# Kernel tuning notes

Measured on AMD Instinct MI355X. Metric: run time of the kernel, lower is better.

The kernel has to match this reference:

```python
import jax, jax.numpy as jnp
import numpy as np

N = 50000   # nodes
F = 32      # num_node_features
EMB = 32    # embedding_size
R = 8       # num_relations
L = 5       # num_layers
E = 400000  # edges


def setup_inputs() -> dict:
    key = jax.random.key(0)
    ks = jax.random.split(key, 12)
    s = 0.1  # weight scale ~ 1/sqrt(fan_in) for stability over 5 residual layers
    return {
        "x": jax.random.normal(ks[0], (N, F), jnp.float32),
        "edge_index": jax.random.randint(ks[1], (2, E), 0, N, jnp.int32),
        "edge_type": jax.random.randint(ks[2], (E,), 0, R, jnp.int32),
        "edge_dist": jax.random.uniform(ks[3], (E,), jnp.float32),
        "fc_W": jax.random.normal(ks[4], (F, EMB), jnp.float32) * s,
        "fc_b": jnp.zeros((EMB,), jnp.float32),
        "rgcn_W": jax.random.normal(ks[5], (L, R, EMB, EMB), jnp.float32) * s,
        "rgcn_root": jax.random.normal(ks[6], (L, EMB, EMB), jnp.float32) * s,
        "rgcn_bias": jnp.zeros((L, EMB), jnp.float32),
        "mlp_W1": jax.random.normal(ks[7], (1 + R, EMB), jnp.float32) * s,
        "mlp_b1": jnp.zeros((EMB,), jnp.float32),
        "mlp_W2": jax.random.normal(ks[8], (EMB, EMB * EMB), jnp.float32) * s,
        "mlp_b2": jnp.zeros((EMB * EMB,), jnp.float32),
        "nn_root": jax.random.normal(ks[9], (L, EMB, EMB), jnp.float32) * s,
        "nn_bias": jnp.zeros((L, EMB), jnp.float32),
    }


def _forward(x, edge_index, edge_type, edge_dist, fc_W, fc_b, rgcn_W, rgcn_root,
             rgcn_bias, mlp_W1, mlp_b1, mlp_W2, mlp_b2, nn_root, nn_bias):
    n = x.shape[0]
    src, dst = edge_index[0], edge_index[1]  # source_to_target flow

    # edge_attr_c = [distance, onehot(edge_type)] : [E, 1+R]
    onehot = jax.nn.one_hot(edge_type, R, dtype=x.dtype)
    eattr = jnp.concatenate([edge_dist[:, None], onehot], axis=1)

    # Shared edge_mlp -> per-edge [EMB, EMB] weight (same for every NNConv layer)
    We = (jax.nn.relu(eattr @ mlp_W1 + mlp_b1) @ mlp_W2 + mlp_b2).reshape(-1, EMB, EMB)

    # degree for NNConv mean aggregation
    deg = jax.ops.segment_sum(jnp.ones_like(edge_dist), dst, num_segments=n)
    denom = jnp.maximum(deg, 1.0)[:, None]

    # per-relation in-degree for RGCN per-relation mean
    rel_cnt = []
    for r in range(R):
        c = jax.ops.segment_sum((edge_type == r).astype(x.dtype), dst, num_segments=n)
        rel_cnt.append(jnp.maximum(c, 1.0)[:, None])

    h = jax.nn.relu(x @ fc_W + fc_b)
    for l in range(L):
        # RGCNConv: root transform + per-relation mean of W_r x_j
        out = h @ rgcn_root[l] + rgcn_bias[l]
        for r in range(R):
            mask_r = (edge_type == r).astype(h.dtype)[:, None]
            msg = (h @ rgcn_W[l, r])[src] * mask_r  # [E, EMB]
            out = out + jax.ops.segment_sum(msg, dst, num_segments=n) / rel_cnt[r]
        h_disc = jax.nn.relu(out)

        # NNConv: x_j @ Theta(e) per edge, mean-aggregated, + root + bias
        msg = jnp.einsum('ei,eio->eo', h[src], We)  # [E, EMB]
        agg = jax.ops.segment_sum(msg, dst, num_segments=n) / denom
        h_cont = jax.nn.relu(h @ nn_root[l] + agg + nn_bias[l])

        h = h + h_disc + h_cont
    return h


def reference(x, edge_index, edge_type, edge_dist, fc_W, fc_b, rgcn_W, rgcn_root,
              rgcn_bias, mlp_W1, mlp_b1, mlp_W2, mlp_b2, nn_root, nn_bias):
    return _forward(x, edge_index, edge_type, edge_dist, fc_W, fc_b, rgcn_W,
                    rgcn_root, rgcn_bias, mlp_W1, mlp_b1, mlp_W2, mlp_b2,
                    nn_root, nn_bias)
```

## Files before the change

### kernel.cpp

```cpp
#include <hip/hip_runtime.h>

#define N_NODES 50000
#define N_EDGES 400000
#define EMB 32
#define NREL 8
#define NLAYER 5
#define NPB 16
#define NBLK (N_NODES / NPB)
#define KROWS 43
#define NCHUNK 196
#define E2CAP (N_EDGES + 8 * N_NODES)

typedef __attribute__((ext_vector_type(8))) short short8;
typedef __attribute__((ext_vector_type(4))) float f32x4;
typedef __attribute__((ext_vector_type(4))) unsigned int u32x4v;

__device__ __forceinline__ unsigned short f2bf(float f) {
    unsigned u = __float_as_uint(f);
    unsigned r = u + 0x7FFF + ((u >> 16) & 1);
    return (unsigned short)(r >> 16);
}

__device__ __forceinline__ unsigned cvt_pk(float a, float b) {
    unsigned r;
    asm("v_cvt_pk_bf16_f32 %0, %1, %2" : "=v"(r) : "v"(a), "v"(b));
    return r;
}

__device__ __forceinline__ int pdeg_of(int d) {
    return (d > 0 ? d + 7 : 8) & ~7;
}

__device__ __forceinline__ int bkt_of(int d) {
    int b = pdeg_of(d) >> 3;
    return (b > 32 ? 32 : b) - 1;
}


__global__ __launch_bounds__(256) void fill_kernel(int* __restrict__ zeroblk,
                                                   float* __restrict__ ha,
                                                   float* __restrict__ hb) {
    int i = blockIdx.x * 256 + threadIdx.x;
    if (i < 10 * N_NODES + 64) zeroblk[i] = 0;
    if (i < EMB) { ha[(size_t)N_NODES * EMB + i] = 0.0f; hb[(size_t)N_NODES * EMB + i] = 0.0f; }
}

__global__ __launch_bounds__(256) void hist_kernel(const int* __restrict__ ei,
                                                   const int* __restrict__ et,
                                                   int* __restrict__ deg,
                                                   int* __restrict__ relcnt) {
    int e = blockIdx.x * 256 + threadIdx.x;
    if (e < N_EDGES) {
        int d = ei[N_EDGES + e];
        atomicAdd(&deg[d], 1);
        atomicAdd(&relcnt[d * NREL + et[e]], 1);
    }
}

__global__ __launch_bounds__(256) void nodeprep_kernel(const int* __restrict__ deg,
                                                       const int* __restrict__ relcnt,
                                                       int* __restrict__ bsum,
                                                       float* __restrict__ invdeg,
                                                       float* __restrict__ invcnt,
                                                       int* __restrict__ bcnt) {
    __shared__ int wsum[4];
    __shared__ int lhist[32];
    int tid = threadIdx.x, lane = tid & 63, wv = tid >> 6;
    if (tid < 32) lhist[tid] = 0;
    int i = blockIdx.x * 256 + tid;
    int d = (i < N_NODES) ? deg[i] : 0;
    int v = (i < N_NODES) ? pdeg_of(d) : 0;
    #pragma unroll
    for (int off = 32; off > 0; off >>= 1) v += __shfl_down(v, off, 64);
    if (lane == 0) wsum[wv] = v;
    __syncthreads();
    if (tid == 0) bsum[blockIdx.x] = wsum[0] + wsum[1] + wsum[2] + wsum[3];
    if (i < N_NODES) {
        invdeg[i] = 1.0f / (float)(d > 0 ? d : 1);
        #pragma unroll
        for (int r = 0; r < NREL; r++) {
            int c = relcnt[i * NREL + r];
            invcnt[i * NREL + r] = 1.0f / (float)(c > 0 ? c : 1);
        }
        atomicAdd(&lhist[bkt_of(d)], 1);
    }
    __syncthreads();
    if (tid < 32 && lhist[tid] > 0) atomicAdd(&bcnt[tid], lhist[tid]);
}

__global__ __launch_bounds__(256) void boff_kernel(const int* __restrict__ bsum,
                                                   int* __restrict__ boff,
                                                   int* __restrict__ row_ptr,
                                                   const int* __restrict__ bcnt,
                                                   int* __restrict__ bcur) {
    __shared__ int ws[4];
    int tid = threadIdx.x, lane = tid & 63, w = tid >> 6;
    int v = (tid < NCHUNK) ? bsum[tid] : 0;
    int incl = v;
    #pragma unroll
    for (int off = 1; off < 64; off <<= 1) {
        int t = __shfl_up(incl, off, 64);
        if (lane >= off) incl += t;
    }
    if (lane == 63) ws[w] = incl;
    __syncthreads();
    int add = 0;
    for (int j = 0; j < w; j++) add += ws[j];
    if (tid < NCHUNK) boff[tid] = add + incl - v;
    if (tid == 0) {
        row_ptr[N_NODES] = ws[0] + ws[1] + ws[2] + ws[3];
        int acc = 0;
        for (int b = 0; b < 32; b++) { bcur[b] = acc; acc += bcnt[b]; }
    }
}

__global__ __launch_bounds__(256) void rptr_kernel(const int* __restrict__ deg,
                                                   const int* __restrict__ boff,
                                                   int* __restrict__ row_ptr,
                                                   int* __restrict__ bcur,
                                                   int* __restrict__ sched) {
    __shared__ int ws[4];
    __shared__ int lcnt[32];
    __shared__ int lbase[32];
    int tid = threadIdx.x, lane = tid & 63, w = tid >> 6;
    if (tid < 32) lcnt[tid] = 0;
    int i = blockIdx.x * 256 + tid;
    int d = (i < N_NODES) ? deg[i] : 0;
    int v = (i < N_NODES) ? pdeg_of(d) : 0;
    int incl = v;
    #pragma unroll
    for (int off = 1; off < 64; off <<= 1) {
        int t = __shfl_up(incl, off, 64);
        if (lane >= off) incl += t;
    }
    if (lane == 63) ws[w] = incl;
    __syncthreads();
    int add = boff[blockIdx.x];
    for (int j = 0; j < w; j++) add += ws[j];
    int rank = 0, bkt = 0;
    if (i < N_NODES) {
        row_ptr[i] = add + incl - v;
        bkt = bkt_of(d);
        rank = atomicAdd(&lcnt[bkt], 1);
    }
    __syncthreads();
    if (tid < 32 && lcnt[tid] > 0) lbase[tid] = atomicAdd(&bcur[tid], lcnt[tid]);
    __syncthreads();
    if (i < N_NODES) sched[lbase[bkt] + rank] = i;
}

__global__ __launch_bounds__(256) void scatter_kernel(const int* __restrict__ ei,
                                                      const int* __restrict__ et,
                                                      const float* __restrict__ ed,
                                                      const int* __restrict__ row_ptr,
                                                      const int* __restrict__ deg,
                                                      int* __restrict__ cursor,
                                                      int2* __restrict__ edge2,
                                                      const int* __restrict__ sched,
                                                      int4* __restrict__ wavetab) {
    int e = blockIdx.x * 256 + threadIdx.x;
    if (e < N_EDGES) {
        int d = ei[N_EDGES + e];
        int pos = row_ptr[d] + atomicAdd(&cursor[d], 1);
        edge2[pos] = make_int2(ei[e] | (et[e] << 16), __float_as_int(ed[e]));
    }
    if (e < N_NODES) {
        int base = row_ptr[e], d = deg[e], pd = pdeg_of(d);
        for (int p = base + d; p < base + pd; ++p)
            edge2[p] = make_int2(N_NODES, 0);
        int node = sched[e];
        wavetab[e] = make_int4(node, row_ptr[node], pdeg_of(deg[node]), 0);
    }
}

__global__ __launch_bounds__(256) void wtbf_kernel(const float* __restrict__ W2,
                                                   const float* __restrict__ b2,
                                                   const float* __restrict__ rgcnW,
                                                   const float* __restrict__ rgcnRoot,
                                                   const float* __restrict__ nnRoot,
                                                   unsigned short* __restrict__ WB) {
    int m = blockIdx.x;
    const float* src;
    if (m < 32) src = W2 + (size_t)m * 1024;
    else if (m == 32) src = b2;
    else {
        int t = m - 33, l = t / 10, j = t % 10;
        src = (j < 8) ? rgcnW + (size_t)(l * 8 + j) * 1024
            : (j == 8) ? rgcnRoot + (size_t)l * 1024
                       : nnRoot + (size_t)l * 1024;
    }
    unsigned short* dst = WB + (size_t)m * 1024;
    #pragma unroll
    for (int c = 0; c < 4; c++) {
        int idx = c * 256 + threadIdx.x;
        int o = idx >> 5, k = idx & 31;
        int i = (k >> 1) + ((k & 1) << 4);
        dst[o * 32 + k] = f2bf(src[i * 32 + o]);
    }
}


__global__ __launch_bounds__(256) void fc_kernel(const float* __restrict__ x,
                                                 const float* __restrict__ W,
                                                 const float* __restrict__ b,
                                                 float* __restrict__ h) {
    __shared__ __align__(16) float xt[8][EMB];
    int tid = threadIdx.x;
    int nl = tid >> 5, lane = tid & 31;
    int n0 = blockIdx.x * 8;
    xt[tid >> 5][tid & 31] = x[n0 * EMB + tid];
    __syncthreads();
    float acc = b[lane];
    #pragma unroll
    for (int i = 0; i < EMB; i++) acc += xt[nl][i] * W[i * EMB + lane];
    int ol = ((lane & 15) << 1) | (lane >> 4);
    h[(n0 + nl) * EMB + ol] = fmaxf(acc, 0.0f);
}


__device__ __forceinline__ void gath(const float* __restrict__ h, int4 E, int m,
                                     float2& ga, float2& gb) {
    ga = *(const float2*)&h[((E.x & 0xFFFF) << 5) + 2 * m];
    gb = *(const float2*)&h[((E.z & 0xFFFF) << 5) + 2 * m];
}

__device__ __forceinline__ void proc_pair(int4 E, float2 ga, float2 gb,
                                          const float2* wrb2f, float w10_0, float w10_1,
                                          unsigned selm, int m,
                                          unsigned& A0s, unsigned& A1s, unsigned& ASs,
                                          unsigned& B0s, unsigned& B1s) {
    int ra = (E.x >> 16) & 7, rb = (E.z >> 16) & 7;
    float2 wa = wrb2f[ra * 16 + m];
    float2 wb = wrb2f[rb * 16 + m];
    float da = __int_as_float(E.y), db = __int_as_float(E.w);
    float hA0 = fmaxf(fmaf(da, w10_0, wa.x), 0.f);
    float hA1 = fmaxf(fmaf(da, w10_1, wa.y), 0.f);
    float hB0 = fmaxf(fmaf(db, w10_0, wb.x), 0.f);
    float hB1 = fmaxf(fmaf(db, w10_1, wb.y), 0.f);
    A0s = cvt_pk(hA0, hB0);
    A1s = cvt_pk(hA1, hB1);
    ASs = cvt_pk((float)((selm >> ra) & 1u), (float)((selm >> rb) & 1u));
    B0s = cvt_pk(ga.x, gb.x);
    B1s = cvt_pk(ga.y, gb.y);
}

__device__ __forceinline__ void mfma6(const unsigned* fa0v, const unsigned* fa1v,
                                      const unsigned* fasv, const unsigned* fb0v,
                                      const unsigned* fb1v,
                                      f32x4& aP00, f32x4& aP01, f32x4& aP10, f32x4& aP11,
                                      f32x4& aS0, f32x4& aS1) {
    u32x4v u0 = {fa0v[0], fa0v[1], fa0v[2], fa0v[3]};
    u32x4v u1 = {fa1v[0], fa1v[1], fa1v[2], fa1v[3]};
    u32x4v us = {fasv[0], fasv[1], fasv[2], fasv[3]};
    u32x4v v0 = {fb0v[0], fb0v[1], fb0v[2], fb0v[3]};
    u32x4v v1 = {fb1v[0], fb1v[1], fb1v[2], fb1v[3]};
    short8 A0 = __builtin_bit_cast(short8, u0);
    short8 A1 = __builtin_bit_cast(short8, u1);
    short8 AS = __builtin_bit_cast(short8, us);
    short8 B0 = __builtin_bit_cast(short8, v0);
    short8 B1 = __builtin_bit_cast(short8, v1);
    aP00 = __builtin_amdgcn_mfma_f32_16x16x32_bf16(A0, B0, aP00, 0, 0, 0);
    aP01 = __builtin_amdgcn_mfma_f32_16x16x32_bf16(A0, B1, aP01, 0, 0, 0);
    aP10 = __builtin_amdgcn_mfma_f32_16x16x32_bf16(A1, B0, aP10, 0, 0, 0);
    aP11 = __builtin_amdgcn_mfma_f32_16x16x32_bf16(A1, B1, aP11, 0, 0, 0);
    aS0  = __builtin_amdgcn_mfma_f32_16x16x32_bf16(AS, B0, aS0, 0, 0, 0);
    aS1  = __builtin_amdgcn_mfma_f32_16x16x32_bf16(AS, B1, aS1, 0, 0, 0);
}

__device__ __forceinline__ void edge_pass(const float* __restrict__ h,
                                          const int2* __restrict__ edge2,
                                          const float2* wrb2f,
                                          int pb, int pe, int quad, int m,
                                          float w10_0, float w10_1, unsigned selm,
                                          int4 E0, float2 g0a, float2 g0b,
                                          f32x4& aP00, f32x4& aP01, f32x4& aP10,
                                          f32x4& aP11, f32x4& aS0, f32x4& aS1) {
    {
        unsigned fa0v[4] = {0,0,0,0}, fa1v[4] = {0,0,0,0}, fasv[4] = {0,0,0,0};
        unsigned fb0v[4] = {0,0,0,0}, fb1v[4] = {0,0,0,0};
        proc_pair(E0, g0a, g0b, wrb2f, w10_0, w10_1, selm, m,
                  fa0v[0], fa1v[0], fasv[0], fb0v[0], fb1v[0]);
        if (pb + 8 < pe) {
            int4 E = *(const int4*)&edge2[pb + 8 + quad * 2];
            float2 ga, gb; gath(h, E, m, ga, gb);
            proc_pair(E, ga, gb, wrb2f, w10_0, w10_1, selm, m,
                      fa0v[1], fa1v[1], fasv[1], fb0v[1], fb1v[1]);
        }
        if (pb + 16 < pe) {
            int4 E = *(const int4*)&edge2[pb + 16 + quad * 2];
            float2 ga, gb; gath(h, E, m, ga, gb);
            proc_pair(E, ga, gb, wrb2f, w10_0, w10_1, selm, m,
                      fa0v[2], fa1v[2], fasv[2], fb0v[2], fb1v[2]);
        }
        if (pb + 24 < pe) {
            int4 E = *(const int4*)&edge2[pb + 24 + quad * 2];
            float2 ga, gb; gath(h, E, m, ga, gb);
            proc_pair(E, ga, gb, wrb2f, w10_0, w10_1, selm, m,
                      fa0v[3], fa1v[3], fasv[3], fb0v[3], fb1v[3]);
        }
        mfma6(fa0v, fa1v, fasv, fb0v, fb1v, aP00, aP01, aP10, aP11, aS0, aS1);
    }
    for (int c0 = pb + 32; c0 < pe; c0 += 32) {
        unsigned fa0v[4] = {0,0,0,0}, fa1v[4] = {0,0,0,0}, fasv[4] = {0,0,0,0};
        unsigned fb0v[4] = {0,0,0,0}, fb1v[4] = {0,0,0,0};
        #pragma unroll
        for (int jp = 0; jp < 4; ++jp) {
            if (c0 + jp * 8 < pe) {
                int4 E = *(const int4*)&edge2[c0 + jp * 8 + quad * 2];
                float2 ga, gb; gath(h, E, m, ga, gb);
                proc_pair(E, ga, gb, wrb2f, w10_0, w10_1, selm, m,
                          fa0v[jp], fa1v[jp], fasv[jp], fb0v[jp], fb1v[jp]);
            }
        }
        mfma6(fa0v, fa1v, fasv, fb0v, fb1v, aP00, aP01, aP10, aP11, aS0, aS1);
    }
}

__device__ __forceinline__ void stage_node(unsigned short (*P)[EMB], int quad, int m,
                                           float idg, const float* __restrict__ invcnt_n,
                                           const float* __restrict__ hrow,
                                           const f32x4& aP00, const f32x4& aP01,
                                           const f32x4& aP10, const f32x4& aP11,
                                           const f32x4& aS0, const f32x4& aS1) {
    #pragma unroll
    for (int reg = 0; reg < 4; ++reg) {
        const int row = quad * 4 + reg;
        *(unsigned*)&P[row][2 * m]      = cvt_pk(aP00[reg] * idg, aP01[reg] * idg);
        *(unsigned*)&P[row + 16][2 * m] = cvt_pk(aP10[reg] * idg, aP11[reg] * idg);
        if (row <= 8) {
            const float sc = (row == 0) ? idg : invcnt_n[row - 1];
            *(unsigned*)&P[32 + row][2 * m] = cvt_pk(aS0[reg] * sc, aS1[reg] * sc);
        }
    }
    if (quad < 2) {
        float2 hh = *(const float2*)&hrow[2 * m];
        *(unsigned*)&P[41 + quad][2 * m] = cvt_pk(hh.x, hh.y);
    }
}

__global__ __launch_bounds__(1024, 8) void layer_kernel(
    const float* __restrict__ h,
    const int2* __restrict__ edge2,
    const int4* __restrict__ wavetab,
    const float* __restrict__ invdeg,
    const float* __restrict__ invcnt,
    const float* __restrict__ W1,
    const float* __restrict__ b1,
    const unsigned short* __restrict__ WBs,
    const unsigned short* __restrict__ WBl,
    const float* __restrict__ rgcnBias_l,
    const float* __restrict__ nnBias_l,
    float* __restrict__ hout,
    int last)
{
    __shared__ __align__(16) unsigned short P_lds[NPB][KROWS][EMB];
    __shared__ __align__(16) float2 wrb2f[NREL * 16];
    __shared__ int nodeid[NPB];

    const int tid = threadIdx.x;

    if (tid < 128) {
        int r = tid >> 4, mi = tid & 15;
        wrb2f[r * 16 + mi] = make_float2(W1[(1 + r) * EMB + mi] + b1[mi],
                                         W1[(1 + r) * EMB + mi + 16] + b1[mi + 16]);
    }

    const int l    = tid & 63;
    const int w    = tid >> 6;
    const int quad = l >> 4;
    const int m    = l & 15;
    const float w10_0 = W1[m];
    const float w10_1 = W1[m + 16];
    const unsigned selm = (m == 0) ? 0xFFu : (m <= 8 ? (1u << (m - 1)) : 0u);

    int4 wt = wavetab[blockIdx.x * NPB + w];
    const int node = wt.x, pb = wt.y, pe = wt.y + wt.z;
    if (l == 0) nodeid[w] = node;
    int4 E0 = *(const int4*)&edge2[pb + quad * 2];
    float2 g0a, g0b;
    gath(h, E0, m, g0a, g0b);

    __syncthreads();

    {
        f32x4 aP00 = {0,0,0,0}, aP01 = {0,0,0,0}, aP10 = {0,0,0,0}, aP11 = {0,0,0,0};
        f32x4 aS0 = {0,0,0,0}, aS1 = {0,0,0,0};
        edge_pass(h, edge2, wrb2f, pb, pe, quad, m, w10_0, w10_1, selm,
                  E0, g0a, g0b, aP00, aP01, aP10, aP11, aS0, aS1);
        stage_node(P_lds[w], quad, m, invdeg[node], invcnt + (size_t)node * NREL,
                   h + (size_t)node * EMB, aP00, aP01, aP10, aP11, aS0, aS1);
    }
    __syncthreads();

    const int node16 = l & 15;
    const int o0 = l & 15;

    f32x4 accN0 = {0,0,0,0}, accN1 = {0,0,0,0};
    f32x4 accR0 = {0,0,0,0}, accR1 = {0,0,0,0};

    #pragma unroll
    for (int j = 0; j < 3; j++) {
        const int rr = w + 16 * j;
        if (rr < KROWS) {
            const unsigned short* Bsrc = (rr < 33) ? (WBs + (size_t)rr * 1024)
                                                   : (WBl + (size_t)(rr - 33) * 1024);
            short8 bf0 = *(const short8*)(Bsrc + o0 * 32 + quad * 8);
            short8 bf1 = *(const short8*)(Bsrc + (o0 + 16) * 32 + quad * 8);
            short8 a = *(const short8*)&P_lds[node16][rr][quad * 8];
            if (rr <= 32 || rr == 42) {
                accN0 = __builtin_amdgcn_mfma_f32_16x16x32_bf16(a, bf0, accN0, 0, 0, 0);
                accN1 = __builtin_amdgcn_mfma_f32_16x16x32_bf16(a, bf1, accN1, 0, 0, 0);
            } else {
                accR0 = __builtin_amdgcn_mfma_f32_16x16x32_bf16(a, bf0, accR0, 0, 0, 0);
                accR1 = __builtin_amdgcn_mfma_f32_16x16x32_bf16(a, bf1, accR1, 0, 0, 0);
            }
        }
    }
    __syncthreads();

    float* RedAll = (float*)&P_lds[0][0][0];
    if (w < 8) {
        float* my = RedAll + w * 1024;
        #pragma unroll
        for (int reg = 0; reg < 4; reg++) {
            int nd = quad * 4 + reg;
            my[nd * 32 + o0]            = accN0[reg];
            my[nd * 32 + o0 + 16]       = accN1[reg];
            my[512 + nd * 32 + o0]      = accR0[reg];
            my[512 + nd * 32 + o0 + 16] = accR1[reg];
        }
    }
    __syncthreads();
    if (w >= 8) {
        float* my = RedAll + (w - 8) * 1024;
        #pragma unroll
        for (int reg = 0; reg < 4; reg++) {
            int nd = quad * 4 + reg;
            my[nd * 32 + o0]            += accN0[reg];
            my[nd * 32 + o0 + 16]       += accN1[reg];
            my[512 + nd * 32 + o0]      += accR0[reg];
            my[512 + nd * 32 + o0 + 16] += accR1[reg];
        }
    }
    __syncthreads();

    if (tid < 512) {
        const int hw2 = tid >> 5, lane = tid & 31;
        const int n2 = nodeid[hw2];
        float sn = 0.0f, sr = 0.0f;
        #pragma unroll
        for (int ww = 0; ww < 8; ww++) {
            sn += RedAll[ww * 1024 + tid];
            sr += RedAll[ww * 1024 + 512 + tid];
        }
        const int il = ((lane & 15) << 1) | (lane >> 4);
        float hd = h[(size_t)n2 * EMB + il];
        float o_r = fmaxf(sr + rgcnBias_l[lane], 0.0f);
        float o_n = fmaxf(sn + nnBias_l[lane], 0.0f);
        hout[(size_t)n2 * EMB + (last ? lane : il)] = hd + o_r + o_n;
    }
}


extern "C" void kernel_launch(void* const* d_in, const int* in_sizes, int n_in,
                              void* d_out, int out_size, void* d_ws, size_t ws_size,
                              hipStream_t stream) {
    const float* x        = (const float*)d_in[0];
    const int*   ei       = (const int*)d_in[1];
    const int*   et       = (const int*)d_in[2];
    const float* ed       = (const float*)d_in[3];
    const float* fcW      = (const float*)d_in[4];
    const float* fcb      = (const float*)d_in[5];
    const float* rgcnW    = (const float*)d_in[6];
    const float* rgcnRoot = (const float*)d_in[7];
    const float* rgcnBias = (const float*)d_in[8];
    const float* W1       = (const float*)d_in[9];
    const float* b1       = (const float*)d_in[10];
    const float* W2       = (const float*)d_in[11];
    const float* b2       = (const float*)d_in[12];
    const float* nnRoot   = (const float*)d_in[13];
    const float* nnBias   = (const float*)d_in[14];

    float* ws = (float*)d_ws;
    float* h_a    = ws;  ws += (size_t)(N_NODES + 1) * EMB;
    float* h_b    = ws;  ws += (size_t)(N_NODES + 1) * EMB;
    float* invdeg = ws;  ws += (size_t)N_NODES;
    float* invcnt = ws;  ws += (size_t)N_NODES * NREL;
    unsigned short* WB = (unsigned short*)ws;  ws += (size_t)83 * 1024 / 2;
    int2* edge2   = (int2*)ws;     ws += (size_t)E2CAP * 2;
    int* row_ptr  = (int*)ws;      ws += (size_t)(N_NODES + 1);
    int* bsum     = (int*)ws;      ws += (size_t)NCHUNK;
    int* boff     = (int*)ws;      ws += (size_t)NCHUNK;
    int* deg      = (int*)ws;      ws += (size_t)N_NODES;
    int* relcnt   = (int*)ws;      ws += (size_t)N_NODES * NREL;
    int* cursor   = (int*)ws;      ws += (size_t)N_NODES;
    int* bcnt     = (int*)ws;      ws += 32;
    int* bcur     = (int*)ws;      ws += 32;
    int* sched    = (int*)ws;      ws += (size_t)N_NODES;
    int4* wavetab = (int4*)ws;     ws += (size_t)N_NODES * 4;
    (void)in_sizes; (void)n_in; (void)out_size; (void)ws_size;

    fill_kernel<<<(10 * N_NODES + 64 + 255) / 256, 256, 0, stream>>>(deg, h_a, h_b);
    hist_kernel<<<(N_EDGES + 255) / 256, 256, 0, stream>>>(ei, et, deg, relcnt);
    nodeprep_kernel<<<NCHUNK, 256, 0, stream>>>(deg, relcnt, bsum, invdeg, invcnt, bcnt);
    boff_kernel<<<1, 256, 0, stream>>>(bsum, boff, row_ptr, bcnt, bcur);
    rptr_kernel<<<NCHUNK, 256, 0, stream>>>(deg, boff, row_ptr, bcur, sched);
    scatter_kernel<<<(N_EDGES + 255) / 256, 256, 0, stream>>>(ei, et, ed, row_ptr, deg,
                                                              cursor, edge2, sched, wavetab);
    wtbf_kernel<<<83, 256, 0, stream>>>(W2, b2, rgcnW, rgcnRoot, nnRoot, WB);
    fc_kernel<<<N_NODES / 8, 256, 0, stream>>>(x, fcW, fcb, h_a);

    const float* hin = h_a;
    float* houtb = h_b;
    for (int l = 0; l < NLAYER; l++) {
        float* dst = (l == NLAYER - 1) ? (float*)d_out : houtb;
        layer_kernel<<<NBLK, 1024, 0, stream>>>(
            hin, edge2, wavetab, invdeg, invcnt, W1, b1,
            WB, WB + (size_t)(33 + l * 10) * 1024,
            rgcnBias + (size_t)l * EMB,
            nnBias + (size_t)l * EMB,
            dst, (l == NLAYER - 1) ? 1 : 0);
        float* old_in = (float*)hin;
        hin = dst;
        houtb = old_in;
    }
}
```

Before: 458.6 us.

## Process two nodes per wave with 512-thread blocks and padded LDS stride

Each layer block now runs 8 waves instead of 16, and each wave handles the edge pass and staging for two nodes. The per-block wave table packs both nodes' ids, padded degrees and row offsets into one int4. The LDS staging buffer gets a padded per-node stride to reduce bank conflicts. The K-row MFMA loop is spread over 8 waves, which removes one reduction pass and one barrier. The aim is better latency hiding through two independent gather streams per wave and less block-level synchronization, at the cost of fewer waves per block and serialized per-node edge work inside each wave.

```diff
diff --git a/kernel.cpp b/kernel.cpp
--- a/kernel.cpp
+++ b/kernel.cpp
@@ -8,6 +8,7 @@
 #define NPB 16
 #define NBLK (N_NODES / NPB)
 #define KROWS 43
+#define PSTRIDE (KROWS * EMB + 8)
 #define NCHUNK 196
 #define E2CAP (N_EDGES + 8 * N_NODES)
 
@@ -168,8 +169,14 @@
         int base = row_ptr[e], d = deg[e], pd = pdeg_of(d);
         for (int p = base + d; p < base + pd; ++p)
             edge2[p] = make_int2(N_NODES, 0);
-        int node = sched[e];
-        wavetab[e] = make_int4(node, row_ptr[node], pdeg_of(deg[node]), 0);
+    }
+    if (e < NBLK * 8) {
+        int b = e >> 3, wv = e & 7;
+        int nA = sched[b * NPB + wv];
+        int nB = sched[b * NPB + 8 + wv];
+        int pbA = row_ptr[nA], pdA = row_ptr[nA + 1] - pbA;
+        int pbB = row_ptr[nB], pdB = row_ptr[nB + 1] - pbB;
+        wavetab[e] = make_int4(nA | ((pdA >> 3) << 20), nB | ((pdB >> 3) << 20), pbA, pbB);
     }
 }
 
@@ -316,7 +323,7 @@
     }
 }
 
-__device__ __forceinline__ void stage_node(unsigned short (*P)[EMB], int quad, int m,
+__device__ __forceinline__ void stage_node(unsigned short* __restrict__ P, int quad, int m,
                                            float idg, const float* __restrict__ invcnt_n,
                                            const float* __restrict__ hrow,
                                            const f32x4& aP00, const f32x4& aP01,
@@ -325,20 +332,20 @@
     #pragma unroll
     for (int reg = 0; reg < 4; ++reg) {
         const int row = quad * 4 + reg;
-        *(unsigned*)&P[row][2 * m]      = cvt_pk(aP00[reg] * idg, aP01[reg] * idg);
-        *(unsigned*)&P[row + 16][2 * m] = cvt_pk(aP10[reg] * idg, aP11[reg] * idg);
+        *(unsigned*)&P[row * EMB + 2 * m]        = cvt_pk(aP00[reg] * idg, aP01[reg] * idg);
+        *(unsigned*)&P[(row + 16) * EMB + 2 * m] = cvt_pk(aP10[reg] * idg, aP11[reg] * idg);
         if (row <= 8) {
             const float sc = (row == 0) ? idg : invcnt_n[row - 1];
-            *(unsigned*)&P[32 + row][2 * m] = cvt_pk(aS0[reg] * sc, aS1[reg] * sc);
+            *(unsigned*)&P[(32 + row) * EMB + 2 * m] = cvt_pk(aS0[reg] * sc, aS1[reg] * sc);
         }
     }
     if (quad < 2) {
         float2 hh = *(const float2*)&hrow[2 * m];
-        *(unsigned*)&P[41 + quad][2 * m] = cvt_pk(hh.x, hh.y);
-    }
-}
-
-__global__ __launch_bounds__(1024, 8) void layer_kernel(
+        *(unsigned*)&P[(41 + quad) * EMB + 2 * m] = cvt_pk(hh.x, hh.y);
+    }
+}
+
+__global__ __launch_bounds__(512, 6) void layer_kernel(
     const float* __restrict__ h,
     const int2* __restrict__ edge2,
     const int4* __restrict__ wavetab,
@@ -353,7 +360,7 @@
     float* __restrict__ hout,
     int last)
 {
-    __shared__ __align__(16) unsigned short P_lds[NPB][KROWS][EMB];
+    __shared__ __align__(16) unsigned short P_lds[NPB * PSTRIDE];
     __shared__ __align__(16) float2 wrb2f[NREL * 16];
     __shared__ int nodeid[NPB];
 
@@ -373,22 +380,36 @@
     const float w10_1 = W1[m + 16];
     const unsigned selm = (m == 0) ? 0xFFu : (m <= 8 ? (1u << (m - 1)) : 0u);
 
-    int4 wt = wavetab[blockIdx.x * NPB + w];
-    const int node = wt.x, pb = wt.y, pe = wt.y + wt.z;
-    if (l == 0) nodeid[w] = node;
-    int4 E0 = *(const int4*)&edge2[pb + quad * 2];
-    float2 g0a, g0b;
+    int4 wt = wavetab[blockIdx.x * 8 + w];
+    const int nA = wt.x & 0xFFFFF, nB = wt.y & 0xFFFFF;
+    const int pbA = wt.z, peA = wt.z + (int)(((unsigned)wt.x >> 20) << 3);
+    const int pbB = wt.w, peB = wt.w + (int)(((unsigned)wt.y >> 20) << 3);
+    if (l == 0) { nodeid[w] = nA; nodeid[w + 8] = nB; }
+    int4 E0 = *(const int4*)&edge2[pbA + quad * 2];
+    int4 E1 = *(const int4*)&edge2[pbB + quad * 2];
+    float2 g0a, g0b, g1a, g1b;
     gath(h, E0, m, g0a, g0b);
+    gath(h, E1, m, g1a, g1b);
 
     __syncthreads();
 
     {
         f32x4 aP00 = {0,0,0,0}, aP01 = {0,0,0,0}, aP10 = {0,0,0,0}, aP11 = {0,0,0,0};
         f32x4 aS0 = {0,0,0,0}, aS1 = {0,0,0,0};
-        edge_pass(h, edge2, wrb2f, pb, pe, quad, m, w10_0, w10_1, selm,
+        edge_pass(h, edge2, wrb2f, pbA, peA, quad, m, w10_0, w10_1, selm,
                   E0, g0a, g0b, aP00, aP01, aP10, aP11, aS0, aS1);
-        stage_node(P_lds[w], quad, m, invdeg[node], invcnt + (size_t)node * NREL,
-                   h + (size_t)node * EMB, aP00, aP01, aP10, aP11, aS0, aS1);
+        stage_node(P_lds + (size_t)w * PSTRIDE, quad, m, invdeg[nA],
+                   invcnt + (size_t)nA * NREL, h + (size_t)nA * EMB,
+                   aP00, aP01, aP10, aP11, aS0, aS1);
+    }
+    {
+        f32x4 aP00 = {0,0,0,0}, aP01 = {0,0,0,0}, aP10 = {0,0,0,0}, aP11 = {0,0,0,0};
+        f32x4 aS0 = {0,0,0,0}, aS1 = {0,0,0,0};
+        edge_pass(h, edge2, wrb2f, pbB, peB, quad, m, w10_0, w10_1, selm,
+                  E1, g1a, g1b, aP00, aP01, aP10, aP11, aS0, aS1);
+        stage_node(P_lds + (size_t)(w + 8) * PSTRIDE, quad, m, invdeg[nB],
+                   invcnt + (size_t)nB * NREL, h + (size_t)nB * EMB,
+                   aP00, aP01, aP10, aP11, aS0, aS1);
     }
     __syncthreads();
 
@@ -399,14 +420,14 @@
     f32x4 accR0 = {0,0,0,0}, accR1 = {0,0,0,0};
 
     #pragma unroll
-    for (int j = 0; j < 3; j++) {
-        const int rr = w + 16 * j;
+    for (int j = 0; j < 6; j++) {
+        const int rr = w + 8 * j;
         if (rr < KROWS) {
             const unsigned short* Bsrc = (rr < 33) ? (WBs + (size_t)rr * 1024)
                                                    : (WBl + (size_t)(rr - 33) * 1024);
             short8 bf0 = *(const short8*)(Bsrc + o0 * 32 + quad * 8);
             short8 bf1 = *(const short8*)(Bsrc + (o0 + 16) * 32 + quad * 8);
-            short8 a = *(const short8*)&P_lds[node16][rr][quad * 8];
+            short8 a = *(const short8*)&P_lds[node16 * PSTRIDE + rr * EMB + quad * 8];
             if (rr <= 32 || rr == 42) {
                 accN0 = __builtin_amdgcn_mfma_f32_16x16x32_bf16(a, bf0, accN0, 0, 0, 0);
                 accN1 = __builtin_amdgcn_mfma_f32_16x16x32_bf16(a, bf1, accN1, 0, 0, 0);
@@ -418,8 +439,8 @@
     }
     __syncthreads();
 
-    float* RedAll = (float*)&P_lds[0][0][0];
-    if (w < 8) {
+    float* RedAll = (float*)&P_lds[0];
+    {
         float* my = RedAll + w * 1024;
         #pragma unroll
         for (int reg = 0; reg < 4; reg++) {
@@ -431,20 +452,8 @@
         }
     }
     __syncthreads();
-    if (w >= 8) {
-        float* my = RedAll + (w - 8) * 1024;
-        #pragma unroll
-        for (int reg = 0; reg < 4; reg++) {
-            int nd = quad * 4 + reg;
-            my[nd * 32 + o0]            += accN0[reg];
-            my[nd * 32 + o0 + 16]       += accN1[reg];
-            my[512 + nd * 32 + o0]      += accR0[reg];
-            my[512 + nd * 32 + o0 + 16] += accR1[reg];
-        }
-    }
-    __syncthreads();
-
-    if (tid < 512) {
+
+    {
         const int hw2 = tid >> 5, lane = tid & 31;
         const int n2 = nodeid[hw2];
         float sn = 0.0f, sr = 0.0f;
@@ -497,7 +506,7 @@
     int* bcnt     = (int*)ws;      ws += 32;
     int* bcur     = (int*)ws;      ws += 32;
     int* sched    = (int*)ws;      ws += (size_t)N_NODES;
-    int4* wavetab = (int4*)ws;     ws += (size_t)N_NODES * 4;
+    int4* wavetab = (int4*)ws;     ws += (size_t)NBLK * 8 * 4;
     (void)in_sizes; (void)n_in; (void)out_size; (void)ws_size;
 
     fill_kernel<<<(10 * N_NODES + 64 + 255) / 256, 256, 0, stream>>>(deg, h_a, h_b);
@@ -514,7 +523,7 @@
     float* houtb = h_b;
     for (int l = 0; l < NLAYER; l++) {
         float* dst = (l == NLAYER - 1) ? (float*)d_out : houtb;
-        layer_kernel<<<NBLK, 1024, 0, stream>>>(
+        layer_kernel<<<NBLK, 512, 0, stream>>>(
             hin, edge2, wavetab, invdeg, invcnt, W1, b1,
             WB, WB + (size_t)(33 + l * 10) * 1024,
             rgcnBias + (size_t)l * EMB,
```

Result: faster. 441.7 us (-3.7%).
